# Performance work log

Hardware: AMD Instinct MI355X
Metric: run time of the kernel (lower is better)

## Reference

```python
import jax, jax.numpy as jnp
import numpy as np

B, L, D, H = 2, 2048, 1024, 16
DH = D // H


def setup_inputs() -> dict:
    key = jax.random.key(0)
    ks = jax.random.split(key, 12)
    s = 0.02
    return {
        "q": jax.random.normal(ks[0], (B, L, D), jnp.float32),
        "k": jax.random.normal(ks[1], (B, L, D), jnp.float32),
        "v": jax.random.normal(ks[2], (B, L, D), jnp.float32),
        "pos_enc": jax.random.normal(ks[3], (L + 1, D), jnp.float32),
        "Wq": jax.random.normal(ks[4], (D, D), jnp.float32) * s,
        "bq": jnp.zeros((D,), jnp.float32),
        "Wk": jax.random.normal(ks[5], (D, D), jnp.float32) * s,
        "bk": jnp.zeros((D,), jnp.float32),
        "Wv": jax.random.normal(ks[6], (D, D), jnp.float32) * s,
        "bv": jnp.zeros((D,), jnp.float32),
        "Wo": jax.random.normal(ks[7], (D, D), jnp.float32) * s,
        "bo": jnp.zeros((D,), jnp.float32),
        "r_w_bias": jax.random.normal(ks[8], (H, 1, DH), jnp.float32) * s,
        "r_r_bias": jax.random.normal(ks[9], (H, 1, DH), jnp.float32) * s,
        "r_kernel": jax.random.normal(ks[10], (H, D, DH), jnp.float32) * s,
    }


def reference(q, k, v, pos_enc, Wq, bq, Wk, bk, Wv, bv, Wo, bo,
              r_w_bias, r_r_bias, r_kernel):
    b, lq, d = q.shape
    h, _, dh = r_w_bias.shape
    lk = k.shape[1]
    scale = dh ** -0.5

    # q/k/v projections, then split heads: [b, l, d] -> [b, h, l, dh]
    qh = (q @ Wq + bq).reshape(b, lq, h, dh).transpose(0, 2, 1, 3)
    kh = (k @ Wk + bk).reshape(b, lk, h, dh).transpose(0, 2, 1, 3)
    vh = (v @ Wv + bv).reshape(b, lk, h, dh).transpose(0, 2, 1, 3)

    # content scores with global content bias (Transformer-XL r_w_bias)
    scores = jnp.einsum('bhqd,bhkd->bhqk', qh + r_w_bias, kh) * scale

    # relative-position term: pos_enc [p, d] @ r_kernel [h, d, dh] -> [h, p, dh]
    pe = jnp.einsum('pd,hde->hpe', pos_enc, r_kernel)
    rel = jnp.einsum('bhqd,hpd->bhqp', qh + r_r_bias, pe) * scale  # [b,h,lq,p]
    p = rel.shape[-1]
    shift = 1 + (lq != lk)
    # rel-shift trick: reshape with swapped last two dims, drop first `shift`
    # rows, reshape back, keep first lk columns
    rel = rel.reshape(b, h, p, lq)[:, :, shift:, :]
    rel = rel.reshape(b, h, lq, p - shift)[..., :lk]
    scores = scores + rel

    # causal mask (key_cache is None path): subtract 1e7 on strict upper triangle
    causal_mask = jnp.triu(jnp.ones((lq, lk), dtype=bool), 1)
    scores = scores - causal_mask * 1e7

    out = jnp.einsum('bhqk,bhkd->bhqd', jax.nn.softmax(scores, axis=-1), vh)
    out = out.transpose(0, 2, 1, 3).reshape(b, lq, d)  # merge heads
    return out @ Wo + bo
```

## Files before the change

kernel.cpp:

```cpp
#include <hip/hip_runtime.h>
#include <hip/hip_bf16.h>

typedef __attribute__((ext_vector_type(8))) short bf16x8;
typedef __attribute__((ext_vector_type(4))) float f32x4;
typedef __attribute__((ext_vector_type(16))) float f32x16;
typedef unsigned short u16;
typedef unsigned int u32;

#define DEV static __device__ __forceinline__

DEV u16 f2us(float x) {
  __hip_bfloat16 h = __float2bfloat16(x);
  union { __hip_bfloat16 h; u16 u; } c; c.h = h; return c.u;
}
DEV float us2f(u16 u) {
  union { __hip_bfloat16 h; u16 u; } c; c.u = u;
  return __bfloat162float(c.h);
}
DEV f32x16 mfma32(bf16x8 a, bf16x8 b, f32x16 c) {
  return __builtin_amdgcn_mfma_f32_32x32x16_bf16(a, b, c, 0, 0, 0);
}

constexpr int PE_ROWS = 2096;
constexpr int PE_M    = 2176;

constexpr size_t SZ_QKV  = (size_t)4096 * 1024 * 2;
constexpr size_t SZ_W    = (size_t)1024 * 1024 * 2;
constexpr size_t SZ_POSB = (size_t)PE_M * 1024 * 2;
constexpr size_t OFF_QB   = 0;
constexpr size_t OFF_KB   = OFF_QB  + SZ_QKV;
constexpr size_t OFF_VB   = OFF_KB  + SZ_QKV;
constexpr size_t OFF_WQT  = OFF_VB  + SZ_QKV;
constexpr size_t OFF_WKT  = OFF_WQT + SZ_W;
constexpr size_t OFF_WVT  = OFF_WKT + SZ_W;
constexpr size_t OFF_WOT  = OFF_WVT + SZ_W;
constexpr size_t OFF_RKT  = OFF_WOT + SZ_W;
constexpr size_t OFF_POSB = OFF_RKT + SZ_W;
constexpr size_t OFF_QW   = OFF_POSB + SZ_POSB;
constexpr size_t OFF_QR   = OFF_QW  + SZ_QKV;
constexpr size_t OFF_KH   = OFF_QR  + SZ_QKV;
constexpr size_t OFF_VT   = OFF_KH  + SZ_QKV;
constexpr size_t OFF_PEH  = OFF_VT  + SZ_QKV;
constexpr size_t OFF_ATTNB = OFF_QB;

__global__ __launch_bounds__(256)
void k_f2b4z(const float4* __restrict__ in, u16* __restrict__ out, int n4in, int n4tot) {
  int i = blockIdx.x * 256 + threadIdx.x;
  if (i >= n4tot) return;
  float4 v;
  if (i < n4in) v = in[i];
  else { v.x = v.y = v.z = v.w = 0.f; }
  ushort4 o;
  o.x = f2us(v.x); o.y = f2us(v.y); o.z = f2us(v.z); o.w = f2us(v.w);
  *reinterpret_cast<ushort4*>(out + (size_t)i * 4) = o;
}

__global__ __launch_bounds__(256)
void k_tconv(const float* __restrict__ in, u16* __restrict__ out) {
  __shared__ float t[32][33];
  const int kb0 = blockIdx.x * 32, nb0 = blockIdx.y * 32;
  const int tx = threadIdx.x & 31, ty = threadIdx.x >> 5;
#pragma unroll
  for (int r = 0; r < 32; r += 8)
    t[ty + r][tx] = in[(size_t)(kb0 + ty + r) * 1024 + nb0 + tx];
  __syncthreads();
#pragma unroll
  for (int r = 0; r < 32; r += 8)
    out[(size_t)(nb0 + ty + r) * 1024 + kb0 + tx] = f2us(t[tx][ty + r]);
}

__global__ __launch_bounds__(256)
void k_rkt(const float* __restrict__ rk, u16* __restrict__ out) {
  __shared__ float t[32][33];
  const int h = blockIdx.z;
  const int eb0 = blockIdx.x * 32, db0 = blockIdx.y * 32;
  const int tx = threadIdx.x & 31, ty = threadIdx.x >> 5;
#pragma unroll
  for (int r = 0; r < 32; r += 8)
    t[ty + r][tx] = rk[(size_t)h * 65536 + (size_t)(db0 + ty + r) * 64 + eb0 + tx];
  __syncthreads();
#pragma unroll
  for (int r = 0; r < 32; r += 8)
    out[(size_t)(h * 64 + eb0 + ty + r) * 1024 + db0 + tx] = f2us(t[tx][ty + r]);
}

struct ProjPtrs {
  const u16 *A0, *A1, *A2, *A3;
  const u16 *B0, *B1, *B2, *B3;
  const float *bias0, *bias1, *bias2;
  const float *rwb, *rrb;
  u16 *Qw, *Qr, *Kh, *Vt, *PEh;
};

__global__ __launch_bounds__(256)
void k_gemm_proj(ProjPtrs pp)
{
  const int z = blockIdx.z;
  if (z == 3 && blockIdx.y >= PE_M / 128) return;
  const u16* A  = (z == 0) ? pp.A0 : (z == 1) ? pp.A1 : (z == 2) ? pp.A2 : pp.A3;
  const u16* Bt = (z == 0) ? pp.B0 : (z == 1) ? pp.B1 : (z == 2) ? pp.B2 : pp.B3;

  __shared__ __attribute__((aligned(16))) u16 As[128][40];
  __shared__ __attribute__((aligned(16))) u16 Bs[128][40];
  const int tid  = threadIdx.x;
  const int lane = tid & 63;
  const int wave = tid >> 6;
  const int bm = blockIdx.y * 128;
  const int bn = blockIdx.x * 128;
  const int wr = (wave >> 1) * 64;
  const int wc = (wave & 1) * 64;
  const int fr = lane & 15;
  const int fk = (lane >> 4) * 8;
  const int srow = tid >> 2;
  const int skb  = (tid & 3) * 8;

  f32x4 zero = {0.f, 0.f, 0.f, 0.f};
  f32x4 acc[4][4];
#pragma unroll
  for (int m = 0; m < 4; ++m)
#pragma unroll
    for (int n = 0; n < 4; ++n) acc[m][n] = zero;

  const u16* pa = A  + (size_t)(bm + srow) * 1024 + skb;
  const u16* pb = Bt + (size_t)(bn + srow) * 1024 + skb;

  for (int k0 = 0; k0 < 1024; k0 += 32) {
    *(bf16x8*)(&As[srow][skb])      = *(const bf16x8*)(pa + k0);
    *(bf16x8*)(&As[srow + 64][skb]) = *(const bf16x8*)(pa + (size_t)64 * 1024 + k0);
    *(bf16x8*)(&Bs[srow][skb])      = *(const bf16x8*)(pb + k0);
    *(bf16x8*)(&Bs[srow + 64][skb]) = *(const bf16x8*)(pb + (size_t)64 * 1024 + k0);
    __syncthreads();
    bf16x8 af[4], bfv[4];
#pragma unroll
    for (int m = 0; m < 4; ++m) af[m]  = *(const bf16x8*)(&As[wr + m * 16 + fr][fk]);
#pragma unroll
    for (int n = 0; n < 4; ++n) bfv[n] = *(const bf16x8*)(&Bs[wc + n * 16 + fr][fk]);
#pragma unroll
    for (int m = 0; m < 4; ++m)
#pragma unroll
      for (int n = 0; n < 4; ++n)
        acc[m][n] = __builtin_amdgcn_mfma_f32_16x16x32_bf16(af[m], bfv[n], acc[m][n], 0, 0, 0);
    __syncthreads();
  }

#pragma unroll
  for (int m = 0; m < 4; ++m)
#pragma unroll
    for (int n = 0; n < 4; ++n)
#pragma unroll
      for (int r = 0; r < 4; ++r) {
        const int grow = bm + wr + m * 16 + (lane >> 4) * 4 + r;
        const int gcol = bn + wc + n * 16 + fr;
        float v = acc[m][n][r];
        const int b_ = grow >> 11, l_ = grow & 2047;
        const int h_ = gcol >> 6,  e_ = gcol & 63;
        if (z == 0) {
          v += pp.bias0[gcol];
          const size_t o = (((size_t)(b_ * 16 + h_) * 2048 + l_) << 6) + e_;
          pp.Qw[o] = f2us(v + pp.rwb[gcol]);
          pp.Qr[o] = f2us(v + pp.rrb[gcol]);
        } else if (z == 1) {
          v += pp.bias1[gcol];
          const size_t o = (((size_t)(b_ * 16 + h_) * 2048 + l_) << 6) + e_;
          pp.Kh[o] = f2us(v);
        } else if (z == 2) {
          v += pp.bias2[gcol];
          const size_t o = (((size_t)(b_ * 16 + h_) * 64 + e_) << 11) + l_;
          pp.Vt[o] = f2us(v);
        } else {
          if (grow < PE_ROWS) {
            const size_t o = ((size_t)h_ * PE_ROWS + grow) * 64 + e_;
            pp.PEh[o] = f2us(v);
          }
        }
      }
}

__global__ __launch_bounds__(256)
void k_gemm_o(const u16* __restrict__ A, const u16* __restrict__ Bt,
              const float* __restrict__ bias, float* __restrict__ outf)
{
  __shared__ __attribute__((aligned(16))) u16 As[128][40];
  __shared__ __attribute__((aligned(16))) u16 Bs[128][40];
  const int tid  = threadIdx.x;
  const int lane = tid & 63;
  const int wave = tid >> 6;
  const int bm = blockIdx.y * 128;
  const int bn = blockIdx.x * 128;
  const int wr = (wave >> 1) * 64;
  const int wc = (wave & 1) * 64;
  const int fr = lane & 15;
  const int fk = (lane >> 4) * 8;
  const int srow = tid >> 2;
  const int skb  = (tid & 3) * 8;

  f32x4 zero = {0.f, 0.f, 0.f, 0.f};
  f32x4 acc[4][4];
#pragma unroll
  for (int m = 0; m < 4; ++m)
#pragma unroll
    for (int n = 0; n < 4; ++n) acc[m][n] = zero;

  const u16* pa = A  + (size_t)(bm + srow) * 1024 + skb;
  const u16* pb = Bt + (size_t)(bn + srow) * 1024 + skb;

  for (int k0 = 0; k0 < 1024; k0 += 32) {
    *(bf16x8*)(&As[srow][skb])      = *(const bf16x8*)(pa + k0);
    *(bf16x8*)(&As[srow + 64][skb]) = *(const bf16x8*)(pa + (size_t)64 * 1024 + k0);
    *(bf16x8*)(&Bs[srow][skb])      = *(const bf16x8*)(pb + k0);
    *(bf16x8*)(&Bs[srow + 64][skb]) = *(const bf16x8*)(pb + (size_t)64 * 1024 + k0);
    __syncthreads();
    bf16x8 af[4], bfv[4];
#pragma unroll
    for (int m = 0; m < 4; ++m) af[m]  = *(const bf16x8*)(&As[wr + m * 16 + fr][fk]);
#pragma unroll
    for (int n = 0; n < 4; ++n) bfv[n] = *(const bf16x8*)(&Bs[wc + n * 16 + fr][fk]);
#pragma unroll
    for (int m = 0; m < 4; ++m)
#pragma unroll
      for (int n = 0; n < 4; ++n)
        acc[m][n] = __builtin_amdgcn_mfma_f32_16x16x32_bf16(af[m], bfv[n], acc[m][n], 0, 0, 0);
    __syncthreads();
  }

#pragma unroll
  for (int m = 0; m < 4; ++m)
#pragma unroll
    for (int n = 0; n < 4; ++n)
#pragma unroll
      for (int r = 0; r < 4; ++r) {
        const int grow = bm + wr + m * 16 + (lane >> 4) * 4 + r;
        const int gcol = bn + wc + n * 16 + fr;
        outf[(size_t)grow * 1024 + gcol] = acc[m][n][r] + bias[gcol];
      }
}

__global__ __launch_bounds__(256, 2)
void k_attn(const u16* __restrict__ Qw, const u16* __restrict__ Qr,
            const u16* __restrict__ Kh, const u16* __restrict__ Vt,
            const u16* __restrict__ PEh, u16* __restrict__ attnb)
{
  const int jb = blockIdx.x, h = blockIdx.y, b = blockIdx.z;
  const int wave = threadIdx.x >> 6, lane = threadIdx.x & 63;
  const int l31 = lane & 31, hi = lane >> 5;
  const int qt = (wave == 0) ? 2 * jb : (wave == 1) ? 2 * jb + 1
               : (wave == 2) ? 62 - 2 * jb : 63 - 2 * jb;
  const int q0 = qt * 32;

  const size_t hb = (size_t)(b * 16 + h);
  const u16* Qw_h = Qw + hb * (2048 * 64);
  const u16* Qr_h = Qr + hb * (2048 * 64);
  const u16* K_h  = Kh + hb * (2048 * 64);
  const u16* V_h  = Vt + hb * (64 * 2048);
  const u16* PE_h = PEh + (size_t)h * (PE_ROWS * 64);

  __shared__ float Elds_all[4][32][100];
  float (*Elds)[100] = Elds_all[wave];

  bf16x8 qwf[4], qrf[4];
#pragma unroll
  for (int kk = 0; kk < 4; ++kk) {
    qwf[kk] = *(const bf16x8*)(Qw_h + (size_t)(q0 + l31) * 64 + kk * 16 + hi * 8);
    qrf[kk] = *(const bf16x8*)(Qr_h + (size_t)(q0 + l31) * 64 + kk * 16 + hi * 8);
  }

  const int Jb0 = 2017 - q0;
  f32x16 carry = {};
#pragma unroll
  for (int kk = 0; kk < 4; ++kk) {
    bf16x8 pe = *(const bf16x8*)(PE_h + (size_t)(Jb0 + l31) * 64 + kk * 16 + hi * 8);
    carry = mfma32(pe, qrf[kk], carry);
  }

  f32x16 Oac[2] = {};
  float mrun = -1e30f, ls = 0.f;

  for (int c0 = 0; c0 <= q0 + 31; c0 += 64) {
    const int Jb = Jb0 + c0;
#pragma unroll
    for (int g = 0; g < 4; ++g) {
      float4 w4 = {carry[4 * g], carry[4 * g + 1], carry[4 * g + 2], carry[4 * g + 3]};
      *(float4*)&Elds[l31][g * 8 + hi * 4] = w4;
    }
#pragma unroll
    for (int tau = 1; tau <= 2; ++tau) {
      f32x16 eacc = {};
#pragma unroll
      for (int kk = 0; kk < 4; ++kk) {
        bf16x8 pe = *(const bf16x8*)(PE_h + (size_t)(Jb + tau * 32 + l31) * 64 + kk * 16 + hi * 8);
        eacc = mfma32(pe, qrf[kk], eacc);
      }
#pragma unroll
      for (int g = 0; g < 4; ++g) {
        float4 w4 = {eacc[4 * g], eacc[4 * g + 1], eacc[4 * g + 2], eacc[4 * g + 3]};
        *(float4*)&Elds[l31][tau * 32 + g * 8 + hi * 4] = w4;
      }
      if (tau == 2) carry = eacc;
    }

    const bool act1 = (c0 + 32 <= q0 + 31);
    f32x16 s0 = {}, s1 = {};
#pragma unroll
    for (int kk = 0; kk < 4; ++kk) {
      bf16x8 kf = *(const bf16x8*)(K_h + (size_t)(c0 + l31) * 64 + kk * 16 + hi * 8);
      s0 = mfma32(kf, qwf[kk], s0);
    }
    if (act1) {
#pragma unroll
      for (int kk = 0; kk < 4; ++kk) {
        bf16x8 kf = *(const bf16x8*)(K_h + (size_t)(c0 + 32 + l31) * 64 + kk * 16 + hi * 8);
        s1 = mfma32(kf, qwf[kk], s1);
      }
    }
    const bool mk0 = (c0 + 31 > q0);
    const bool mk1 = (c0 + 63 > q0);
#pragma unroll
    for (int r = 0; r < 16; ++r) {
      const int pat = (r & 3) + 8 * (r >> 2) + 4 * hi;
      float e = Elds[l31][pat + 31 - l31];
      float x = (s0[r] + e) * 0.125f;
      if (mk0 && (c0 + pat > q0 + l31)) x = -1e30f;
      s0[r] = x;
    }
    if (act1) {
#pragma unroll
      for (int r = 0; r < 16; ++r) {
        const int pat = (r & 3) + 8 * (r >> 2) + 4 * hi;
        float e = Elds[l31][32 + pat + 31 - l31];
        float x = (s1[r] + e) * 0.125f;
        if (mk1 && (c0 + 32 + pat > q0 + l31)) x = -1e30f;
        s1[r] = x;
      }
    }
    float mx = s0[0];
#pragma unroll
    for (int r = 1; r < 16; ++r) mx = fmaxf(mx, s0[r]);
    if (act1) {
#pragma unroll
      for (int r = 0; r < 16; ++r) mx = fmaxf(mx, s1[r]);
    }
    mx = fmaxf(mx, __shfl_xor(mx, 32));
    const float mn = fmaxf(mrun, mx);
    const float al = __expf(mrun - mn);
    mrun = mn;

    float rsum = 0.f;
    u32 w0a[8], w1a[8];
#pragma unroll
    for (int g = 0; g < 8; ++g) {
      float pa = __expf(s0[2 * g] - mn);
      float pb = __expf(s0[2 * g + 1] - mn);
      u16 ua = f2us(pa), ub = f2us(pb);
      rsum += us2f(ua) + us2f(ub);
      w0a[g] = (u32)ua | ((u32)ub << 16);
    }
    if (act1) {
#pragma unroll
      for (int g = 0; g < 8; ++g) {
        float pa = __expf(s1[2 * g] - mn);
        float pb = __expf(s1[2 * g + 1] - mn);
        u16 ua = f2us(pa), ub = f2us(pb);
        rsum += us2f(ua) + us2f(ub);
        w1a[g] = (u32)ua | ((u32)ub << 16);
      }
    }
    ls = ls * al + rsum + __shfl_xor(rsum, 32);
    Oac[0] *= al;
    Oac[1] *= al;

#define PV_KT(WARR, KT)                                                        \
    {                                                                          \
      _Pragma("unroll")                                                        \
      for (int kvs = 0; kvs < 2; ++kvs) {                                      \
        u32 snd0 = hi ? WARR[4 * kvs]     : WARR[4 * kvs + 2];                 \
        u32 snd1 = hi ? WARR[4 * kvs + 1] : WARR[4 * kvs + 3];                 \
        u32 r0 = (u32)__shfl_xor((int)snd0, 32);                               \
        u32 r1 = (u32)__shfl_xor((int)snd1, 32);                               \
        union { u32 u[4]; bf16x8 v; } pf;                                      \
        pf.u[0] = hi ? r0 : WARR[4 * kvs];                                     \
        pf.u[1] = hi ? r1 : WARR[4 * kvs + 1];                                 \
        pf.u[2] = hi ? WARR[4 * kvs + 2] : r0;                                 \
        pf.u[3] = hi ? WARR[4 * kvs + 3] : r1;                                 \
        _Pragma("unroll")                                                      \
        for (int dt = 0; dt < 2; ++dt) {                                       \
          bf16x8 vf = *(const bf16x8*)(V_h + (size_t)(dt * 32 + l31) * 2048    \
                                       + c0 + KT * 32 + kvs * 16 + hi * 8);    \
          Oac[dt] = mfma32(vf, pf.v, Oac[dt]);                                 \
        }                                                                      \
      }                                                                        \
    }
    PV_KT(w0a, 0)
    if (act1) PV_KT(w1a, 1)
#undef PV_KT
  }

  const float invl = 1.f / ls;
  const size_t orow = ((size_t)(b * 2048 + q0 + l31)) * 1024 + h * 64;
#pragma unroll
  for (int dt = 0; dt < 2; ++dt)
#pragma unroll
    for (int g = 0; g < 4; ++g) {
      ushort4 st;
      st.x = f2us(Oac[dt][4 * g + 0] * invl);
      st.y = f2us(Oac[dt][4 * g + 1] * invl);
      st.z = f2us(Oac[dt][4 * g + 2] * invl);
      st.w = f2us(Oac[dt][4 * g + 3] * invl);
      *(ushort4*)(attnb + orow + dt * 32 + g * 8 + hi * 4) = st;
    }
}

extern "C" void kernel_launch(void* const* d_in, const int* in_sizes, int n_in,
                              void* d_out, int out_size, void* d_ws, size_t ws_size,
                              hipStream_t stream)
{
  const float* q   = (const float*)d_in[0];
  const float* k   = (const float*)d_in[1];
  const float* v   = (const float*)d_in[2];
  const float* pos = (const float*)d_in[3];
  const float* Wq  = (const float*)d_in[4];
  const float* bq  = (const float*)d_in[5];
  const float* Wk  = (const float*)d_in[6];
  const float* bk  = (const float*)d_in[7];
  const float* Wv  = (const float*)d_in[8];
  const float* bv  = (const float*)d_in[9];
  const float* Wo  = (const float*)d_in[10];
  const float* bo  = (const float*)d_in[11];
  const float* rwb = (const float*)d_in[12];
  const float* rrb = (const float*)d_in[13];
  const float* rk  = (const float*)d_in[14];

  char* ws = (char*)d_ws;
  u16* qb    = (u16*)(ws + OFF_QB);
  u16* kb    = (u16*)(ws + OFF_KB);
  u16* vb    = (u16*)(ws + OFF_VB);
  u16* Wqt   = (u16*)(ws + OFF_WQT);
  u16* Wkt   = (u16*)(ws + OFF_WKT);
  u16* Wvt   = (u16*)(ws + OFF_WVT);
  u16* Wot   = (u16*)(ws + OFF_WOT);
  u16* Rkt   = (u16*)(ws + OFF_RKT);
  u16* posb  = (u16*)(ws + OFF_POSB);
  u16* Qw    = (u16*)(ws + OFF_QW);
  u16* Qr    = (u16*)(ws + OFF_QR);
  u16* Kh    = (u16*)(ws + OFF_KH);
  u16* Vt    = (u16*)(ws + OFF_VT);
  u16* PEh   = (u16*)(ws + OFF_PEH);
  u16* attnb = (u16*)(ws + OFF_ATTNB);
  float* outf = (float*)d_out;

  k_f2b4z<<<dim3(4096), 256, 0, stream>>>((const float4*)q, qb, 1048576, 1048576);
  k_f2b4z<<<dim3(4096), 256, 0, stream>>>((const float4*)k, kb, 1048576, 1048576);
  k_f2b4z<<<dim3(4096), 256, 0, stream>>>((const float4*)v, vb, 1048576, 1048576);
  k_f2b4z<<<dim3(2176), 256, 0, stream>>>((const float4*)pos, posb,
                                          (2049 * 1024) / 4, (PE_M * 1024) / 4);
  k_tconv<<<dim3(32, 32), 256, 0, stream>>>(Wq, Wqt);
  k_tconv<<<dim3(32, 32), 256, 0, stream>>>(Wk, Wkt);
  k_tconv<<<dim3(32, 32), 256, 0, stream>>>(Wv, Wvt);
  k_tconv<<<dim3(32, 32), 256, 0, stream>>>(Wo, Wot);
  k_rkt<<<dim3(2, 32, 16), 256, 0, stream>>>(rk, Rkt);

  ProjPtrs pp;
  pp.A0 = qb;  pp.A1 = kb;  pp.A2 = vb;  pp.A3 = posb;
  pp.B0 = Wqt; pp.B1 = Wkt; pp.B2 = Wvt; pp.B3 = Rkt;
  pp.bias0 = bq; pp.bias1 = bk; pp.bias2 = bv;
  pp.rwb = rwb; pp.rrb = rrb;
  pp.Qw = Qw; pp.Qr = Qr; pp.Kh = Kh; pp.Vt = Vt; pp.PEh = PEh;
  k_gemm_proj<<<dim3(8, 32, 4), 256, 0, stream>>>(pp);

  k_attn<<<dim3(16, 16, 2), 256, 0, stream>>>(Qw, Qr, Kh, Vt, PEh, attnb);

  k_gemm_o<<<dim3(8, 32), 256, 0, stream>>>(attnb, Wot, bo, outf);
}
```

Before: 279.7 us.

## Use direct global-to-LDS loads in GEMMs and restructure attention loads and scheduling

Both GEMM kernels now stage tiles with global_load_lds (16-byte direct-to-LDS loads) into unpadded LDS tiles, so the data no longer passes through registers. The attention kernel switches to a 1D grid remapped so that blocks of the same head land on the same XCD, and it alternates which waves take the long and short query tiles. It also issues all PE, K and V fragment loads at the top of each iteration and always computes the second 32-key subtile instead of branching on it. PE_ROWS grows so those unconditional loads stay in bounds. The unpadded LDS layout risks bank conflicts, and the extra masked work and register pressure may offset the gains from better load overlap.

```diff
diff --git a/kernel.cpp b/kernel.cpp
--- a/kernel.cpp
+++ b/kernel.cpp
@@ -20,8 +20,13 @@
 DEV f32x16 mfma32(bf16x8 a, bf16x8 b, f32x16 c) {
   return __builtin_amdgcn_mfma_f32_32x32x16_bf16(a, b, c, 0, 0, 0);
 }
-
-constexpr int PE_ROWS = 2096;
+DEV void gl16(const u16* g, u16* l) {
+  __builtin_amdgcn_global_load_lds(
+      (const __attribute__((address_space(1))) unsigned int*)(g),
+      (__attribute__((address_space(3))) unsigned int*)(l), 16, 0, 0);
+}
+
+constexpr int PE_ROWS = 2144;
 constexpr int PE_M    = 2176;
 
 constexpr size_t SZ_QKV  = (size_t)4096 * 1024 * 2;
@@ -100,8 +105,8 @@
   const u16* A  = (z == 0) ? pp.A0 : (z == 1) ? pp.A1 : (z == 2) ? pp.A2 : pp.A3;
   const u16* Bt = (z == 0) ? pp.B0 : (z == 1) ? pp.B1 : (z == 2) ? pp.B2 : pp.B3;
 
-  __shared__ __attribute__((aligned(16))) u16 As[128][40];
-  __shared__ __attribute__((aligned(16))) u16 Bs[128][40];
+  __shared__ __attribute__((aligned(16))) u16 As[128 * 32];
+  __shared__ __attribute__((aligned(16))) u16 Bs[128 * 32];
   const int tid  = threadIdx.x;
   const int lane = tid & 63;
   const int wave = tid >> 6;
@@ -111,8 +116,6 @@
   const int wc = (wave & 1) * 64;
   const int fr = lane & 15;
   const int fk = (lane >> 4) * 8;
-  const int srow = tid >> 2;
-  const int skb  = (tid & 3) * 8;
 
   f32x4 zero = {0.f, 0.f, 0.f, 0.f};
   f32x4 acc[4][4];
@@ -121,20 +124,23 @@
 #pragma unroll
     for (int n = 0; n < 4; ++n) acc[m][n] = zero;
 
-  const u16* pa = A  + (size_t)(bm + srow) * 1024 + skb;
-  const u16* pb = Bt + (size_t)(bn + srow) * 1024 + skb;
+  const int cA = wave * 2;
+  const u16* gA = A  + (size_t)(bm + cA * 16 + (lane >> 2)) * 1024 + (lane & 3) * 8;
+  const u16* gB = Bt + (size_t)(bn + cA * 16 + (lane >> 2)) * 1024 + (lane & 3) * 8;
+  u16* lA = As + cA * 512;
+  u16* lB = Bs + cA * 512;
 
   for (int k0 = 0; k0 < 1024; k0 += 32) {
-    *(bf16x8*)(&As[srow][skb])      = *(const bf16x8*)(pa + k0);
-    *(bf16x8*)(&As[srow + 64][skb]) = *(const bf16x8*)(pa + (size_t)64 * 1024 + k0);
-    *(bf16x8*)(&Bs[srow][skb])      = *(const bf16x8*)(pb + k0);
-    *(bf16x8*)(&Bs[srow + 64][skb]) = *(const bf16x8*)(pb + (size_t)64 * 1024 + k0);
+    gl16(gA + k0, lA);
+    gl16(gA + 16 * 1024 + k0, lA + 512);
+    gl16(gB + k0, lB);
+    gl16(gB + 16 * 1024 + k0, lB + 512);
     __syncthreads();
     bf16x8 af[4], bfv[4];
 #pragma unroll
-    for (int m = 0; m < 4; ++m) af[m]  = *(const bf16x8*)(&As[wr + m * 16 + fr][fk]);
-#pragma unroll
-    for (int n = 0; n < 4; ++n) bfv[n] = *(const bf16x8*)(&Bs[wc + n * 16 + fr][fk]);
+    for (int m = 0; m < 4; ++m) af[m]  = *(const bf16x8*)(&As[(wr + m * 16 + fr) * 32 + fk]);
+#pragma unroll
+    for (int n = 0; n < 4; ++n) bfv[n] = *(const bf16x8*)(&Bs[(wc + n * 16 + fr) * 32 + fk]);
 #pragma unroll
     for (int m = 0; m < 4; ++m)
 #pragma unroll
@@ -180,8 +186,8 @@
 void k_gemm_o(const u16* __restrict__ A, const u16* __restrict__ Bt,
               const float* __restrict__ bias, float* __restrict__ outf)
 {
-  __shared__ __attribute__((aligned(16))) u16 As[128][40];
-  __shared__ __attribute__((aligned(16))) u16 Bs[128][40];
+  __shared__ __attribute__((aligned(16))) u16 As[128 * 32];
+  __shared__ __attribute__((aligned(16))) u16 Bs[128 * 32];
   const int tid  = threadIdx.x;
   const int lane = tid & 63;
   const int wave = tid >> 6;
@@ -191,8 +197,6 @@
   const int wc = (wave & 1) * 64;
   const int fr = lane & 15;
   const int fk = (lane >> 4) * 8;
-  const int srow = tid >> 2;
-  const int skb  = (tid & 3) * 8;
 
   f32x4 zero = {0.f, 0.f, 0.f, 0.f};
   f32x4 acc[4][4];
@@ -201,20 +205,23 @@
 #pragma unroll
     for (int n = 0; n < 4; ++n) acc[m][n] = zero;
 
-  const u16* pa = A  + (size_t)(bm + srow) * 1024 + skb;
-  const u16* pb = Bt + (size_t)(bn + srow) * 1024 + skb;
+  const int cA = wave * 2;
+  const u16* gA = A  + (size_t)(bm + cA * 16 + (lane >> 2)) * 1024 + (lane & 3) * 8;
+  const u16* gB = Bt + (size_t)(bn + cA * 16 + (lane >> 2)) * 1024 + (lane & 3) * 8;
+  u16* lA = As + cA * 512;
+  u16* lB = Bs + cA * 512;
 
   for (int k0 = 0; k0 < 1024; k0 += 32) {
-    *(bf16x8*)(&As[srow][skb])      = *(const bf16x8*)(pa + k0);
-    *(bf16x8*)(&As[srow + 64][skb]) = *(const bf16x8*)(pa + (size_t)64 * 1024 + k0);
-    *(bf16x8*)(&Bs[srow][skb])      = *(const bf16x8*)(pb + k0);
-    *(bf16x8*)(&Bs[srow + 64][skb]) = *(const bf16x8*)(pb + (size_t)64 * 1024 + k0);
+    gl16(gA + k0, lA);
+    gl16(gA + 16 * 1024 + k0, lA + 512);
+    gl16(gB + k0, lB);
+    gl16(gB + 16 * 1024 + k0, lB + 512);
     __syncthreads();
     bf16x8 af[4], bfv[4];
 #pragma unroll
-    for (int m = 0; m < 4; ++m) af[m]  = *(const bf16x8*)(&As[wr + m * 16 + fr][fk]);
-#pragma unroll
-    for (int n = 0; n < 4; ++n) bfv[n] = *(const bf16x8*)(&Bs[wc + n * 16 + fr][fk]);
+    for (int m = 0; m < 4; ++m) af[m]  = *(const bf16x8*)(&As[(wr + m * 16 + fr) * 32 + fk]);
+#pragma unroll
+    for (int n = 0; n < 4; ++n) bfv[n] = *(const bf16x8*)(&Bs[(wc + n * 16 + fr) * 32 + fk]);
 #pragma unroll
     for (int m = 0; m < 4; ++m)
 #pragma unroll
@@ -240,18 +247,23 @@
             const u16* __restrict__ Kh, const u16* __restrict__ Vt,
             const u16* __restrict__ PEh, u16* __restrict__ attnb)
 {
-  const int jb = blockIdx.x, h = blockIdx.y, b = blockIdx.z;
+  const int bid = blockIdx.x;
+  const int xcd = bid & 7, slot = bid >> 3;
+  const int jb = slot & 15, g = slot >> 4;
+  const int hb = xcd + 8 * g;
+  const int h = hb & 15, b = hb >> 4;
   const int wave = threadIdx.x >> 6, lane = threadIdx.x & 63;
   const int l31 = lane & 31, hi = lane >> 5;
-  const int qt = (wave == 0) ? 2 * jb : (wave == 1) ? 2 * jb + 1
-               : (wave == 2) ? 62 - 2 * jb : 63 - 2 * jb;
+  const int par = ((slot >> 5) ^ jb) & 1;
+  const int tshort = (wave & 2) ? 2 * jb + 1 : 2 * jb;
+  const int tlong  = (wave & 2) ? 62 - 2 * jb : 63 - 2 * jb;
+  const int qt = ((wave & 1) ^ par) ? tlong : tshort;
   const int q0 = qt * 32;
 
-  const size_t hb = (size_t)(b * 16 + h);
-  const u16* Qw_h = Qw + hb * (2048 * 64);
-  const u16* Qr_h = Qr + hb * (2048 * 64);
-  const u16* K_h  = Kh + hb * (2048 * 64);
-  const u16* V_h  = Vt + hb * (64 * 2048);
+  const u16* Qw_h = Qw + (size_t)hb * (2048 * 64);
+  const u16* Qr_h = Qr + (size_t)hb * (2048 * 64);
+  const u16* K_h  = Kh + (size_t)hb * (2048 * 64);
+  const u16* V_h  = Vt + (size_t)hb * (64 * 2048);
   const u16* PE_h = PEh + (size_t)h * (PE_ROWS * 64);
 
   __shared__ float Elds_all[4][32][100];
@@ -277,68 +289,71 @@
 
   for (int c0 = 0; c0 <= q0 + 31; c0 += 64) {
     const int Jb = Jb0 + c0;
-#pragma unroll
-    for (int g = 0; g < 4; ++g) {
-      float4 w4 = {carry[4 * g], carry[4 * g + 1], carry[4 * g + 2], carry[4 * g + 3]};
-      *(float4*)&Elds[l31][g * 8 + hi * 4] = w4;
-    }
-#pragma unroll
-    for (int tau = 1; tau <= 2; ++tau) {
-      f32x16 eacc = {};
-#pragma unroll
-      for (int kk = 0; kk < 4; ++kk) {
-        bf16x8 pe = *(const bf16x8*)(PE_h + (size_t)(Jb + tau * 32 + l31) * 64 + kk * 16 + hi * 8);
-        eacc = mfma32(pe, qrf[kk], eacc);
+    bf16x8 pe1[4], pe2[4], kf0[4], kf1[4];
+#pragma unroll
+    for (int kk = 0; kk < 4; ++kk) {
+      const int ko = kk * 16 + hi * 8;
+      pe1[kk] = *(const bf16x8*)(PE_h + (size_t)(Jb + 32 + l31) * 64 + ko);
+      pe2[kk] = *(const bf16x8*)(PE_h + (size_t)(Jb + 64 + l31) * 64 + ko);
+      kf0[kk] = *(const bf16x8*)(K_h + (size_t)(c0 + l31) * 64 + ko);
+      kf1[kk] = *(const bf16x8*)(K_h + (size_t)(c0 + 32 + l31) * 64 + ko);
+    }
+    bf16x8 vfr[2][2][2];
+#pragma unroll
+    for (int kt = 0; kt < 2; ++kt)
+#pragma unroll
+      for (int kvs = 0; kvs < 2; ++kvs)
+#pragma unroll
+        for (int dt = 0; dt < 2; ++dt)
+          vfr[kt][kvs][dt] = *(const bf16x8*)(V_h + (size_t)(dt * 32 + l31) * 2048
+                                              + c0 + kt * 32 + kvs * 16 + hi * 8);
+#pragma unroll
+    for (int g4 = 0; g4 < 4; ++g4) {
+      float4 w4 = {carry[4 * g4], carry[4 * g4 + 1], carry[4 * g4 + 2], carry[4 * g4 + 3]};
+      *(float4*)&Elds[l31][g4 * 8 + hi * 4] = w4;
+    }
+    {
+      f32x16 e1 = {}, e2 = {};
+#pragma unroll
+      for (int kk = 0; kk < 4; ++kk) e1 = mfma32(pe1[kk], qrf[kk], e1);
+#pragma unroll
+      for (int kk = 0; kk < 4; ++kk) e2 = mfma32(pe2[kk], qrf[kk], e2);
+#pragma unroll
+      for (int g4 = 0; g4 < 4; ++g4) {
+        float4 w4 = {e1[4 * g4], e1[4 * g4 + 1], e1[4 * g4 + 2], e1[4 * g4 + 3]};
+        *(float4*)&Elds[l31][32 + g4 * 8 + hi * 4] = w4;
       }
 #pragma unroll
-      for (int g = 0; g < 4; ++g) {
-        float4 w4 = {eacc[4 * g], eacc[4 * g + 1], eacc[4 * g + 2], eacc[4 * g + 3]};
-        *(float4*)&Elds[l31][tau * 32 + g * 8 + hi * 4] = w4;
+      for (int g4 = 0; g4 < 4; ++g4) {
+        float4 w4 = {e2[4 * g4], e2[4 * g4 + 1], e2[4 * g4 + 2], e2[4 * g4 + 3]};
+        *(float4*)&Elds[l31][64 + g4 * 8 + hi * 4] = w4;
       }
-      if (tau == 2) carry = eacc;
-    }
-
-    const bool act1 = (c0 + 32 <= q0 + 31);
+      carry = e2;
+    }
     f32x16 s0 = {}, s1 = {};
 #pragma unroll
-    for (int kk = 0; kk < 4; ++kk) {
-      bf16x8 kf = *(const bf16x8*)(K_h + (size_t)(c0 + l31) * 64 + kk * 16 + hi * 8);
-      s0 = mfma32(kf, qwf[kk], s0);
-    }
-    if (act1) {
-#pragma unroll
-      for (int kk = 0; kk < 4; ++kk) {
-        bf16x8 kf = *(const bf16x8*)(K_h + (size_t)(c0 + 32 + l31) * 64 + kk * 16 + hi * 8);
-        s1 = mfma32(kf, qwf[kk], s1);
-      }
-    }
-    const bool mk0 = (c0 + 31 > q0);
-    const bool mk1 = (c0 + 63 > q0);
+    for (int kk = 0; kk < 4; ++kk) s0 = mfma32(kf0[kk], qwf[kk], s0);
+#pragma unroll
+    for (int kk = 0; kk < 4; ++kk) s1 = mfma32(kf1[kk], qwf[kk], s1);
 #pragma unroll
     for (int r = 0; r < 16; ++r) {
       const int pat = (r & 3) + 8 * (r >> 2) + 4 * hi;
       float e = Elds[l31][pat + 31 - l31];
       float x = (s0[r] + e) * 0.125f;
-      if (mk0 && (c0 + pat > q0 + l31)) x = -1e30f;
+      if (c0 + pat > q0 + l31) x = -1e30f;
       s0[r] = x;
     }
-    if (act1) {
-#pragma unroll
-      for (int r = 0; r < 16; ++r) {
-        const int pat = (r & 3) + 8 * (r >> 2) + 4 * hi;
-        float e = Elds[l31][32 + pat + 31 - l31];
-        float x = (s1[r] + e) * 0.125f;
-        if (mk1 && (c0 + 32 + pat > q0 + l31)) x = -1e30f;
-        s1[r] = x;
-      }
-    }
-    float mx = s0[0];
-#pragma unroll
-    for (int r = 1; r < 16; ++r) mx = fmaxf(mx, s0[r]);
-    if (act1) {
-#pragma unroll
-      for (int r = 0; r < 16; ++r) mx = fmaxf(mx, s1[r]);
-    }
+#pragma unroll
+    for (int r = 0; r < 16; ++r) {
+      const int pat = (r & 3) + 8 * (r >> 2) + 4 * hi;
+      float e = Elds[l31][32 + pat + 31 - l31];
+      float x = (s1[r] + e) * 0.125f;
+      if (c0 + 32 + pat > q0 + l31) x = -1e30f;
+      s1[r] = x;
+    }
+    float mx = fmaxf(s0[0], s1[0]);
+#pragma unroll
+    for (int r = 1; r < 16; ++r) mx = fmaxf(mx, fmaxf(s0[r], s1[r]));
     mx = fmaxf(mx, __shfl_xor(mx, 32));
     const float mn = fmaxf(mrun, mx);
     const float al = __expf(mrun - mn);
@@ -347,22 +362,20 @@
     float rsum = 0.f;
     u32 w0a[8], w1a[8];
 #pragma unroll
-    for (int g = 0; g < 8; ++g) {
-      float pa = __expf(s0[2 * g] - mn);
-      float pb = __expf(s0[2 * g + 1] - mn);
+    for (int g8 = 0; g8 < 8; ++g8) {
+      float pa = __expf(s0[2 * g8] - mn);
+      float pb = __expf(s0[2 * g8 + 1] - mn);
       u16 ua = f2us(pa), ub = f2us(pb);
       rsum += us2f(ua) + us2f(ub);
-      w0a[g] = (u32)ua | ((u32)ub << 16);
-    }
-    if (act1) {
-#pragma unroll
-      for (int g = 0; g < 8; ++g) {
-        float pa = __expf(s1[2 * g] - mn);
-        float pb = __expf(s1[2 * g + 1] - mn);
-        u16 ua = f2us(pa), ub = f2us(pb);
-        rsum += us2f(ua) + us2f(ub);
-        w1a[g] = (u32)ua | ((u32)ub << 16);
-      }
+      w0a[g8] = (u32)ua | ((u32)ub << 16);
+    }
+#pragma unroll
+    for (int g8 = 0; g8 < 8; ++g8) {
+      float pa = __expf(s1[2 * g8] - mn);
+      float pb = __expf(s1[2 * g8 + 1] - mn);
+      u16 ua = f2us(pa), ub = f2us(pb);
+      rsum += us2f(ua) + us2f(ub);
+      w1a[g8] = (u32)ua | ((u32)ub << 16);
     }
     ls = ls * al + rsum + __shfl_xor(rsum, 32);
     Oac[0] *= al;
@@ -382,15 +395,12 @@
         pf.u[2] = hi ? WARR[4 * kvs + 2] : r0;                                 \
         pf.u[3] = hi ? WARR[4 * kvs + 3] : r1;                                 \
         _Pragma("unroll")                                                      \
-        for (int dt = 0; dt < 2; ++dt) {                                       \
-          bf16x8 vf = *(const bf16x8*)(V_h + (size_t)(dt * 32 + l31) * 2048    \
-                                       + c0 + KT * 32 + kvs * 16 + hi * 8);    \
-          Oac[dt] = mfma32(vf, pf.v, Oac[dt]);                                 \
-        }                                                                      \
+        for (int dt = 0; dt < 2; ++dt)                                         \
+          Oac[dt] = mfma32(vfr[KT][kvs][dt], pf.v, Oac[dt]);                   \
       }                                                                        \
     }
     PV_KT(w0a, 0)
-    if (act1) PV_KT(w1a, 1)
+    PV_KT(w1a, 1)
 #undef PV_KT
   }
 
@@ -399,13 +409,13 @@
 #pragma unroll
   for (int dt = 0; dt < 2; ++dt)
 #pragma unroll
-    for (int g = 0; g < 4; ++g) {
+    for (int g4 = 0; g4 < 4; ++g4) {
       ushort4 st;
-      st.x = f2us(Oac[dt][4 * g + 0] * invl);
-      st.y = f2us(Oac[dt][4 * g + 1] * invl);
-      st.z = f2us(Oac[dt][4 * g + 2] * invl);
-      st.w = f2us(Oac[dt][4 * g + 3] * invl);
-      *(ushort4*)(attnb + orow + dt * 32 + g * 8 + hi * 4) = st;
+      st.x = f2us(Oac[dt][4 * g4 + 0] * invl);
+      st.y = f2us(Oac[dt][4 * g4 + 1] * invl);
+      st.z = f2us(Oac[dt][4 * g4 + 2] * invl);
+      st.w = f2us(Oac[dt][4 * g4 + 3] * invl);
+      *(ushort4*)(attnb + orow + dt * 32 + g4 * 8 + hi * 4) = st;
     }
 }
 
@@ -466,7 +476,7 @@
   pp.Qw = Qw; pp.Qr = Qr; pp.Kh = Kh; pp.Vt = Vt; pp.PEh = PEh;
   k_gemm_proj<<<dim3(8, 32, 4), 256, 0, stream>>>(pp);
 
-  k_attn<<<dim3(16, 16, 2), 256, 0, stream>>>(Qw, Qr, Kh, Vt, PEh, attnb);
+  k_attn<<<dim3(512), 256, 0, stream>>>(Qw, Qr, Kh, Vt, PEh, attnb);
 
   k_gemm_o<<<dim3(8, 32), 256, 0, stream>>>(attnb, Wot, bo, outf);
 }
```

Result: faster. 266.6 us (-4.7%).
